# Performance work log

Measured on AMD Instinct MI355X. Metric: run time of the kernel, lower is better.

Reference implementation:

```python
import jax, jax.numpy as jnp
import numpy as np

B, T, D, H = 4, 2048, 1024, 16
HD = D // H  # 64


def setup_inputs() -> dict:
    key = jax.random.key(0)
    k1, k2, k3 = jax.random.split(key, 3)
    x = jax.random.normal(k1, (B, T, D), dtype=jnp.float32)
    # xavier-uniform-ish scaling for stability
    W_qkv = jax.random.normal(k2, (3 * D, D), dtype=jnp.float32) * (1.0 / np.sqrt(D))
    W_proj = jax.random.normal(k3, (D, D), dtype=jnp.float32) * (1.0 / np.sqrt(D))
    b_proj = jnp.zeros((D,), dtype=jnp.float32)
    return {"x": x, "W_qkv": W_qkv, "W_proj": W_proj, "b_proj": b_proj}


def reference(x, W_qkv, W_proj, b_proj):
    Bx, Tx, C = x.shape
    qkv = x @ W_qkv.T                      # [B,T,3C]
    q, k, v = jnp.split(qkv, 3, axis=-1)
    # [B,T,C] -> [B,H,T,hd]
    def heads(t):
        return t.reshape(Bx, Tx, H, HD).transpose(0, 2, 1, 3)
    q, k, v = heads(q), heads(k), heads(v)
    scale = 1.0 / np.sqrt(HD)
    scores = jnp.einsum('bhqd,bhkd->bhqk', q, k) * scale  # [B,H,T,T]
    causal = jnp.tril(jnp.ones((Tx, Tx), dtype=bool))
    scores = jnp.where(causal, scores, jnp.finfo(scores.dtype).min)
    attn = jax.nn.softmax(scores, axis=-1)
    out = jnp.einsum('bhqk,bhkd->bhqd', attn, v)          # [B,H,T,hd]
    out = out.transpose(0, 2, 1, 3).reshape(Bx, Tx, C)    # [B,T,C]
    return out @ W_proj.T + b_proj
```

## Files before the change

### kernel.cpp

```cpp
#include <hip/hip_runtime.h>
#include <hip/hip_bf16.h>

#define B_  4
#define T_  2048
#define D_  1024
#define H_  16
#define HD_ 64
#define THREE_D (3 * D_)
#define TWO_D   (2 * D_)

typedef short s16x8 __attribute__((ext_vector_type(8)));
typedef float f32x4 __attribute__((ext_vector_type(4)));
typedef unsigned short u16;
typedef unsigned short u16x4 __attribute__((ext_vector_type(4)));

static __device__ __forceinline__ s16x8 load8(const u16* p) {
    return *reinterpret_cast<const s16x8*>(p);
}
static __device__ __forceinline__ u16 f2bf(float f) {
    __hip_bfloat16 h = __float2bfloat16(f);
    return *reinterpret_cast<u16*>(&h);
}
static __device__ __forceinline__ u16 bftrunc(float f) {
    unsigned u; __builtin_memcpy(&u, &f, 4); return (u16)(u >> 16);
}

static __device__ __forceinline__ void gload_lds16(const u16* g, u16* l) {
#if __has_builtin(__builtin_amdgcn_global_load_lds)
    __builtin_amdgcn_global_load_lds(
        (__attribute__((address_space(1))) void*)g,
        (__attribute__((address_space(3))) void*)l, 16, 0, 0);
#else
    *reinterpret_cast<s16x8*>(l) = load8(g);
#endif
}

__global__ __launch_bounds__(256) void cvt_f32_bf16(
    const float* __restrict__ in, u16* __restrict__ out, int n)
{
    const int i = (blockIdx.x * 256 + threadIdx.x) * 4;
    if (i < n) {
        const float4 f = *reinterpret_cast<const float4*>(in + i);
        u16x4 r;
        r.x = f2bf(f.x); r.y = f2bf(f.y); r.z = f2bf(f.z); r.w = f2bf(f.w);
        *reinterpret_cast<u16x4*>(out + i) = r;
    }
}

template<int MODE>
__global__ __launch_bounds__(256) void gemm_bt128(
    const u16* __restrict__ A,
    const u16* __restrict__ Bm,
    void* __restrict__ Cv,
    const float* __restrict__ bias,
    int M, int N, int K, int lda, int ldb, int ldc,
    float qsc, u16* __restrict__ vt)
{
    const int ntiles = N >> 7;
    const int mt = blockIdx.x / ntiles;
    const int nt = blockIdx.x % ntiles;
    const int m0 = mt * 128, n0 = nt * 128;
    const int tid  = threadIdx.x;
    const int lane = tid & 63;
    const int l15  = lane & 15;
    const int quad = lane >> 4;
    const int wave = tid >> 6;
    const int wm = (wave >> 1) * 64;
    const int wn = (wave & 1) * 64;

    __shared__ u16 A_sh[2][128 * 32];
    __shared__ u16 B_sh[2][128 * 32];

    f32x4 acc[4][4] = {};

    const int c0 = tid, c1 = tid + 256;
    const int ar0 = c0 >> 2, as0 = (c0 & 3) * 8;
    const int ar1 = c1 >> 2, as1 = (c1 & 3) * 8;
    const u16* Ag0 = A  + (size_t)(m0 + ar0) * lda + as0;
    const u16* Ag1 = A  + (size_t)(m0 + ar1) * lda + as1;
    const u16* Bg0 = Bm + (size_t)(n0 + ar0) * ldb + as0;
    const u16* Bg1 = Bm + (size_t)(n0 + ar1) * ldb + as1;

    for (int k0 = 0; k0 < K; k0 += 64) {
        __syncthreads();
        #pragma unroll
        for (int p = 0; p < 2; ++p) {
            gload_lds16(Ag0 + k0 + p * 32, &A_sh[p][c0 * 8]);
            gload_lds16(Ag1 + k0 + p * 32, &A_sh[p][c1 * 8]);
            gload_lds16(Bg0 + k0 + p * 32, &B_sh[p][c0 * 8]);
            gload_lds16(Bg1 + k0 + p * 32, &B_sh[p][c1 * 8]);
        }
        __syncthreads();

        #pragma unroll
        for (int p = 0; p < 2; ++p) {
            s16x8 a[4], b[4];
            #pragma unroll
            for (int i = 0; i < 4; ++i) {
                a[i] = *reinterpret_cast<const s16x8*>(&A_sh[p][(wm + i * 16 + l15) * 32 + quad * 8]);
                b[i] = *reinterpret_cast<const s16x8*>(&B_sh[p][(wn + i * 16 + l15) * 32 + quad * 8]);
            }
            #pragma unroll
            for (int mi = 0; mi < 4; ++mi)
                #pragma unroll
                for (int ni = 0; ni < 4; ++ni)
                    acc[mi][ni] = __builtin_amdgcn_mfma_f32_16x16x32_bf16(
                        a[mi], b[ni], acc[mi][ni], 0, 0, 0);
        }
    }

    #pragma unroll
    for (int ni = 0; ni < 4; ++ni) {
        const int col = n0 + wn + ni * 16 + l15;
        if (MODE == 0) {
            const float bv = bias ? bias[col] : 0.0f;
            #pragma unroll
            for (int mi = 0; mi < 4; ++mi) {
                const int row = m0 + wm + mi * 16 + quad * 4;
                #pragma unroll
                for (int r = 0; r < 4; ++r)
                    ((float*)Cv)[(size_t)(row + r) * ldc + col] = acc[mi][ni][r] + bv;
            }
        } else {
            if (col < TWO_D) {
                const float sc = (col < D_) ? qsc : 1.0f;
                #pragma unroll
                for (int mi = 0; mi < 4; ++mi) {
                    const int row = m0 + wm + mi * 16 + quad * 4;
                    #pragma unroll
                    for (int r = 0; r < 4; ++r)
                        ((u16*)Cv)[(size_t)(row + r) * ldc + col] = f2bf(acc[mi][ni][r] * sc);
                }
            } else {
                const int vc = col - TWO_D;
                #pragma unroll
                for (int mi = 0; mi < 4; ++mi) {
                    const int row = m0 + wm + mi * 16 + quad * 4;
                    const int bb = row >> 11, t = row & (T_ - 1);
                    u16x4 pk;
                    #pragma unroll
                    for (int r = 0; r < 4; ++r) pk[r] = f2bf(acc[mi][ni][r]);
                    *reinterpret_cast<u16x4*>(
                        vt + ((size_t)(bb * H_ * HD_) + vc) * T_ + t) = pk;
                }
            }
        }
    }
}

__global__ __launch_bounds__(256) void flash_attn6(
    const u16* __restrict__ qk, const u16* __restrict__ vt,
    u16* __restrict__ out)
{
    const int cls = blockIdx.x >> 6;
    const int bh  = blockIdx.x & 63;
    const int qmap[16] = {15,14,13,12, 8,9,10,11, 7,6,5,4, 0,1,2,3};
    const int qt = qmap[cls];
    const int h = bh & 15, b = bh >> 4;
    const int q0 = qt * 128;

    __shared__ u16 K_lds[64 * 72];
    __shared__ u16 V_lds[64 * 72];
    __shared__ u16 P_lds[4 * 32 * 72];

    const int tid = threadIdx.x;
    const int wave = tid >> 6, lane = tid & 63;
    const int l15 = lane & 15, quad = lane >> 4;
    u16* Pw = P_lds + wave * (32 * 72);

    const int w0 = q0 + wave * 32;

    s16x8 qf[2][2];
    #pragma unroll
    for (int mi = 0; mi < 2; ++mi) {
        const size_t rowQ = (size_t)(b * T_ + w0 + mi * 16 + l15) * TWO_D + h * HD_;
        qf[mi][0] = load8(qk + rowQ + quad * 8);
        qf[mi][1] = load8(qk + rowQ + 32 + quad * 8);
    }

    f32x4 o[2][4] = {};
    f32x4 osum[2] = {};

    s16x8 ones;
    #pragma unroll
    for (int j = 0; j < 8; ++j) ones[j] = (short)0x3F80;

    const int r0 = tid >> 3;
    const int s0 = (tid & 7) * 8;
    const u16* Kg0 = qk + (size_t)(b * T_ + r0)      * TWO_D + D_ + h * HD_ + s0;
    const u16* Kg1 = qk + (size_t)(b * T_ + r0 + 32) * TWO_D + D_ + h * HD_ + s0;
    const u16* Vg0 = vt + (size_t)(bh * HD_ + r0)      * T_ + s0;
    const u16* Vg1 = vt + (size_t)(bh * HD_ + r0 + 32) * T_ + s0;

    s16x8 pk0 = load8(Kg0);
    s16x8 pk1 = load8(Kg1);
    s16x8 pv0 = load8(Vg0);
    s16x8 pv1 = load8(Vg1);

    const int nkt = 2 * qt + 2;
    for (int kt = 0; kt < nkt; ++kt) {
        const int kbase = kt * 64;
        __syncthreads();
        *reinterpret_cast<s16x8*>(&K_lds[r0 * 72 + s0])        = pk0;
        *reinterpret_cast<s16x8*>(&K_lds[(r0 + 32) * 72 + s0]) = pk1;
        *reinterpret_cast<s16x8*>(&V_lds[r0 * 72 + s0])        = pv0;
        *reinterpret_cast<s16x8*>(&V_lds[(r0 + 32) * 72 + s0]) = pv1;
        __syncthreads();

        if (kt + 1 < nkt) {
            const int nb = kbase + 64;
            pk0 = load8(Kg0 + (size_t)nb * TWO_D);
            pk1 = load8(Kg1 + (size_t)nb * TWO_D);
            pv0 = load8(Vg0 + nb);
            pv1 = load8(Vg1 + nb);
        }

        if (kbase <= w0 + 31) {
            f32x4 st[2][4];
            #pragma unroll
            for (int n = 0; n < 4; ++n) {
                const s16x8 kf0 = *reinterpret_cast<const s16x8*>(
                    &K_lds[(n * 16 + l15) * 72 + quad * 8]);
                const s16x8 kf1 = *reinterpret_cast<const s16x8*>(
                    &K_lds[(n * 16 + l15) * 72 + 32 + quad * 8]);
                #pragma unroll
                for (int mi = 0; mi < 2; ++mi) {
                    f32x4 t = {};
                    t = __builtin_amdgcn_mfma_f32_16x16x32_bf16(kf0, qf[mi][0], t, 0, 0, 0);
                    t = __builtin_amdgcn_mfma_f32_16x16x32_bf16(kf1, qf[mi][1], t, 0, 0, 0);
                    st[mi][n] = t;
                }
            }

            const bool diag = (kbase + 63 > w0);
            #pragma unroll
            for (int mi = 0; mi < 2; ++mi) {
                const int qr = w0 + mi * 16 + l15;
                #pragma unroll
                for (int n = 0; n < 4; ++n) {
                    const int kb = kbase + n * 16 + quad * 4;
                    u16x4 pk;
                    #pragma unroll
                    for (int r = 0; r < 4; ++r)
                        pk[r] = bftrunc(exp2f(st[mi][n][r]));
                    if (diag) {
                        #pragma unroll
                        for (int r = 0; r < 4; ++r)
                            if (kb + r > qr) pk[r] = 0;
                    }
                    *reinterpret_cast<u16x4*>(
                        &Pw[(mi * 16 + l15) * 72 + n * 16 + quad * 4]) = pk;
                }
            }

            #pragma unroll
            for (int ks = 0; ks < 2; ++ks) {
                s16x8 pa[2];
                #pragma unroll
                for (int mi = 0; mi < 2; ++mi) {
                    pa[mi] = *reinterpret_cast<const s16x8*>(
                        &Pw[(mi * 16 + l15) * 72 + ks * 32 + quad * 8]);
                    osum[mi] = __builtin_amdgcn_mfma_f32_16x16x32_bf16(
                        pa[mi], ones, osum[mi], 0, 0, 0);
                }
                #pragma unroll
                for (int n4 = 0; n4 < 4; ++n4) {
                    const s16x8 vb = *reinterpret_cast<const s16x8*>(
                        &V_lds[(n4 * 16 + l15) * 72 + ks * 32 + quad * 8]);
                    #pragma unroll
                    for (int mi = 0; mi < 2; ++mi)
                        o[mi][n4] = __builtin_amdgcn_mfma_f32_16x16x32_bf16(
                            pa[mi], vb, o[mi][n4], 0, 0, 0);
                }
            }
        }
    }

    #pragma unroll
    for (int mi = 0; mi < 2; ++mi)
        #pragma unroll
        for (int r = 0; r < 4; ++r) {
            const float inv = 1.0f / osum[mi][r];
            const size_t rowO = (size_t)(b * T_ + w0 + mi * 16 + quad * 4 + r) * D_ + h * HD_;
            #pragma unroll
            for (int n4 = 0; n4 < 4; ++n4)
                out[rowO + n4 * 16 + l15] = f2bf(o[mi][n4][r] * inv);
        }
}

extern "C" void kernel_launch(void* const* d_in, const int* in_sizes, int n_in,
                              void* d_out, int out_size, void* d_ws, size_t ws_size,
                              hipStream_t stream)
{
    const float* x     = (const float*)d_in[0];
    const float* Wqkv  = (const float*)d_in[1];
    const float* Wproj = (const float*)d_in[2];
    const float* bproj = (const float*)d_in[3];
    float* out = (float*)d_out;

    const int M = B_ * T_;
    const float cs = 0.18033688011f;

    u16* xb    = (u16*)d_ws;
    u16* wqkvb = xb    + (size_t)M * D_;
    u16* wprob = wqkvb + (size_t)THREE_D * D_;
    u16* qk    = wprob + (size_t)D_ * D_;
    u16* vtb   = qk    + (size_t)M * TWO_D;
    u16* attn  = vtb   + (size_t)B_ * H_ * HD_ * T_;

    {
        int n;
        n = M * D_;
        cvt_f32_bf16<<<dim3((n / 4 + 255) / 256), 256, 0, stream>>>(x, xb, n);
        n = THREE_D * D_;
        cvt_f32_bf16<<<dim3((n / 4 + 255) / 256), 256, 0, stream>>>(Wqkv, wqkvb, n);
        n = D_ * D_;
        cvt_f32_bf16<<<dim3((n / 4 + 255) / 256), 256, 0, stream>>>(Wproj, wprob, n);
    }

    gemm_bt128<1><<<dim3((M / 128) * (THREE_D / 128)), 256, 0, stream>>>(
        xb, wqkvb, qk, nullptr, M, THREE_D, D_, D_, D_, TWO_D, cs, vtb);

    flash_attn6<<<dim3(B_ * H_ * (T_ / 128)), 256, 0, stream>>>(qk, vtb, attn);

    gemm_bt128<0><<<dim3((M / 128) * (D_ / 128)), 256, 0, stream>>>(
        attn, wprob, out, bproj, M, D_, D_, D_, D_, D_, 1.0f, nullptr);
}
```

Baseline: 255.6 us.

## Rework attention kernel with 32x32 MFMA, register-resident P, and async double-buffered K/V

```diff
diff --git a/kernel.cpp b/kernel.cpp
--- a/kernel.cpp
+++ b/kernel.cpp
@@ -11,6 +11,8 @@
 
 typedef short s16x8 __attribute__((ext_vector_type(8)));
 typedef float f32x4 __attribute__((ext_vector_type(4)));
+typedef float f32x16 __attribute__((ext_vector_type(16)));
+typedef unsigned int u32x4 __attribute__((ext_vector_type(4)));
 typedef unsigned short u16;
 typedef unsigned short u16x4 __attribute__((ext_vector_type(4)));
 
@@ -21,8 +23,13 @@
     __hip_bfloat16 h = __float2bfloat16(f);
     return *reinterpret_cast<u16*>(&h);
 }
-static __device__ __forceinline__ u16 bftrunc(float f) {
-    unsigned u; __builtin_memcpy(&u, &f, 4); return (u16)(u >> 16);
+static __device__ __forceinline__ unsigned cvtpk(float lo, float hi) {
+    float2 f; f.x = lo; f.y = hi;
+    __hip_bfloat162 h = __float22bfloat162_rn(f);
+    return *reinterpret_cast<unsigned*>(&h);
+}
+static __device__ __forceinline__ void swap32(unsigned& a, unsigned& b) {
+    asm("v_permlane32_swap_b32 %0, %1" : "+v"(a), "+v"(b));
 }
 
 static __device__ __forceinline__ void gload_lds16(const u16* g, u16* l) {
@@ -148,7 +155,7 @@
     }
 }
 
-__global__ __launch_bounds__(256) void flash_attn6(
+__global__ __launch_bounds__(256) void flash_attn7(
     const u16* __restrict__ qk, const u16* __restrict__ vt,
     u16* __restrict__ out)
 {
@@ -156,136 +163,129 @@
     const int bh  = blockIdx.x & 63;
     const int qmap[16] = {15,14,13,12, 8,9,10,11, 7,6,5,4, 0,1,2,3};
     const int qt = qmap[cls];
-    const int h = bh & 15, b = bh >> 4;
+    const int hh = bh & 15, b = bh >> 4;
     const int q0 = qt * 128;
 
-    __shared__ u16 K_lds[64 * 72];
-    __shared__ u16 V_lds[64 * 72];
-    __shared__ u16 P_lds[4 * 32 * 72];
+    __shared__ u16 K_lds[2][64 * 64];
+    __shared__ u16 V_lds[2][64 * 64];
 
     const int tid = threadIdx.x;
     const int wave = tid >> 6, lane = tid & 63;
-    const int l15 = lane & 15, quad = lane >> 4;
-    u16* Pw = P_lds + wave * (32 * 72);
-
+    const int l31 = lane & 31, half = lane >> 5;
+    const int sw = (l31 & 7) << 4;
     const int w0 = q0 + wave * 32;
-
-    s16x8 qf[2][2];
-    #pragma unroll
-    for (int mi = 0; mi < 2; ++mi) {
-        const size_t rowQ = (size_t)(b * T_ + w0 + mi * 16 + l15) * TWO_D + h * HD_;
-        qf[mi][0] = load8(qk + rowQ + quad * 8);
-        qf[mi][1] = load8(qk + rowQ + 32 + quad * 8);
-    }
-
-    f32x4 o[2][4] = {};
-    f32x4 osum[2] = {};
+    const int qr = w0 + l31;
+
+    s16x8 qf[4];
+    {
+        const size_t rowQ = (size_t)(b * T_ + w0 + l31) * TWO_D + hh * HD_;
+        #pragma unroll
+        for (int s = 0; s < 4; ++s)
+            qf[s] = load8(qk + rowQ + s * 16 + half * 8);
+    }
+
+    f32x16 o[2] = {};
+    f32x16 osum = {};
 
     s16x8 ones;
     #pragma unroll
     for (int j = 0; j < 8; ++j) ones[j] = (short)0x3F80;
 
     const int r0 = tid >> 3;
-    const int s0 = (tid & 7) * 8;
-    const u16* Kg0 = qk + (size_t)(b * T_ + r0)      * TWO_D + D_ + h * HD_ + s0;
-    const u16* Kg1 = qk + (size_t)(b * T_ + r0 + 32) * TWO_D + D_ + h * HD_ + s0;
-    const u16* Vg0 = vt + (size_t)(bh * HD_ + r0)      * T_ + s0;
-    const u16* Vg1 = vt + (size_t)(bh * HD_ + r0 + 32) * T_ + s0;
-
-    s16x8 pk0 = load8(Kg0);
-    s16x8 pk1 = load8(Kg1);
-    s16x8 pv0 = load8(Vg0);
-    s16x8 pv1 = load8(Vg1);
+    const int ch = tid & 7;
+    const int scol = ((ch * 16) ^ ((r0 & 7) << 4)) >> 1;
+    const u16* Kg = qk + (size_t)(b * T_ + r0) * TWO_D + D_ + hh * HD_ + scol;
+    const u16* Vg = vt + (size_t)(bh * HD_ + r0) * T_ + scol;
+
+#define STAGE(bf, kb64) do {                                                  \
+        const size_t ko = (size_t)(kb64) * TWO_D;                             \
+        gload_lds16(Kg + ko,                       &K_lds[bf][(size_t)tid * 8]);        \
+        gload_lds16(Kg + ko + (size_t)32 * TWO_D,  &K_lds[bf][(size_t)(tid + 256) * 8]);\
+        gload_lds16(Vg + (kb64),                   &V_lds[bf][(size_t)tid * 8]);        \
+        gload_lds16(Vg + (kb64) + (size_t)32 * T_, &V_lds[bf][(size_t)(tid + 256) * 8]);\
+    } while (0)
 
     const int nkt = 2 * qt + 2;
+    STAGE(0, 0);
+    int cur = 0;
+
     for (int kt = 0; kt < nkt; ++kt) {
         const int kbase = kt * 64;
         __syncthreads();
-        *reinterpret_cast<s16x8*>(&K_lds[r0 * 72 + s0])        = pk0;
-        *reinterpret_cast<s16x8*>(&K_lds[(r0 + 32) * 72 + s0]) = pk1;
-        *reinterpret_cast<s16x8*>(&V_lds[r0 * 72 + s0])        = pv0;
-        *reinterpret_cast<s16x8*>(&V_lds[(r0 + 32) * 72 + s0]) = pv1;
-        __syncthreads();
-
-        if (kt + 1 < nkt) {
-            const int nb = kbase + 64;
-            pk0 = load8(Kg0 + (size_t)nb * TWO_D);
-            pk1 = load8(Kg1 + (size_t)nb * TWO_D);
-            pv0 = load8(Vg0 + nb);
-            pv1 = load8(Vg1 + nb);
+        if (kt + 1 < nkt) STAGE(cur ^ 1, (kt + 1) * 64);
+
+        if (kbase <= w0 + 31) {
+            const char* Kb = (const char*)&K_lds[cur][0];
+            const char* Vb = (const char*)&V_lds[cur][0];
+
+            f32x16 st[2];
+            #pragma unroll
+            for (int kb = 0; kb < 2; ++kb) {
+                f32x16 acc = {};
+                #pragma unroll
+                for (int s = 0; s < 4; ++s) {
+                    const s16x8 kf = *reinterpret_cast<const s16x8*>(
+                        Kb + (kb * 32 + l31) * 128 + ((s * 32 + half * 16) ^ sw));
+                    acc = __builtin_amdgcn_mfma_f32_32x32x16_bf16(
+                        kf, qf[s], acc, 0, 0, 0);
+                }
+                st[kb] = acc;
+            }
+
+            const bool diag = (kbase + 63 > w0);
+            float p[2][16];
+            #pragma unroll
+            for (int kb = 0; kb < 2; ++kb)
+                #pragma unroll
+                for (int r = 0; r < 16; ++r) {
+                    float e = exp2f(st[kb][r]);
+                    if (diag) {
+                        const int key = kbase + kb * 32 + (r & 3) + 8 * (r >> 2) + 4 * half;
+                        if (key > qr) e = 0.0f;
+                    }
+                    p[kb][r] = e;
+                }
+
+            s16x8 pa[4];
+            #pragma unroll
+            for (int kb = 0; kb < 2; ++kb)
+                #pragma unroll
+                for (int t = 0; t < 2; ++t) {
+                    unsigned a  = cvtpk(p[kb][8 * t + 0], p[kb][8 * t + 1]);
+                    unsigned bq = cvtpk(p[kb][8 * t + 4], p[kb][8 * t + 5]);
+                    unsigned c  = cvtpk(p[kb][8 * t + 2], p[kb][8 * t + 3]);
+                    unsigned d  = cvtpk(p[kb][8 * t + 6], p[kb][8 * t + 7]);
+                    swap32(a, bq);
+                    swap32(c, d);
+                    u32x4 w; w.x = a; w.y = c; w.z = bq; w.w = d;
+                    pa[kb * 2 + t] = __builtin_bit_cast(s16x8, w);
+                }
+
+            #pragma unroll
+            for (int s = 0; s < 4; ++s) {
+                osum = __builtin_amdgcn_mfma_f32_32x32x16_bf16(
+                    pa[s], ones, osum, 0, 0, 0);
+                #pragma unroll
+                for (int fb = 0; fb < 2; ++fb) {
+                    const s16x8 vb = *reinterpret_cast<const s16x8*>(
+                        Vb + (fb * 32 + l31) * 128 + ((s * 32 + half * 16) ^ sw));
+                    o[fb] = __builtin_amdgcn_mfma_f32_32x32x16_bf16(
+                        pa[s], vb, o[fb], 0, 0, 0);
+                }
+            }
         }
-
-        if (kbase <= w0 + 31) {
-            f32x4 st[2][4];
-            #pragma unroll
-            for (int n = 0; n < 4; ++n) {
-                const s16x8 kf0 = *reinterpret_cast<const s16x8*>(
-                    &K_lds[(n * 16 + l15) * 72 + quad * 8]);
-                const s16x8 kf1 = *reinterpret_cast<const s16x8*>(
-                    &K_lds[(n * 16 + l15) * 72 + 32 + quad * 8]);
-                #pragma unroll
-                for (int mi = 0; mi < 2; ++mi) {
-                    f32x4 t = {};
-                    t = __builtin_amdgcn_mfma_f32_16x16x32_bf16(kf0, qf[mi][0], t, 0, 0, 0);
-                    t = __builtin_amdgcn_mfma_f32_16x16x32_bf16(kf1, qf[mi][1], t, 0, 0, 0);
-                    st[mi][n] = t;
-                }
-            }
-
-            const bool diag = (kbase + 63 > w0);
-            #pragma unroll
-            for (int mi = 0; mi < 2; ++mi) {
-                const int qr = w0 + mi * 16 + l15;
-                #pragma unroll
-                for (int n = 0; n < 4; ++n) {
-                    const int kb = kbase + n * 16 + quad * 4;
-                    u16x4 pk;
-                    #pragma unroll
-                    for (int r = 0; r < 4; ++r)
-                        pk[r] = bftrunc(exp2f(st[mi][n][r]));
-                    if (diag) {
-                        #pragma unroll
-                        for (int r = 0; r < 4; ++r)
-                            if (kb + r > qr) pk[r] = 0;
-                    }
-                    *reinterpret_cast<u16x4*>(
-                        &Pw[(mi * 16 + l15) * 72 + n * 16 + quad * 4]) = pk;
-                }
-            }
-
-            #pragma unroll
-            for (int ks = 0; ks < 2; ++ks) {
-                s16x8 pa[2];
-                #pragma unroll
-                for (int mi = 0; mi < 2; ++mi) {
-                    pa[mi] = *reinterpret_cast<const s16x8*>(
-                        &Pw[(mi * 16 + l15) * 72 + ks * 32 + quad * 8]);
-                    osum[mi] = __builtin_amdgcn_mfma_f32_16x16x32_bf16(
-                        pa[mi], ones, osum[mi], 0, 0, 0);
-                }
-                #pragma unroll
-                for (int n4 = 0; n4 < 4; ++n4) {
-                    const s16x8 vb = *reinterpret_cast<const s16x8*>(
-                        &V_lds[(n4 * 16 + l15) * 72 + ks * 32 + quad * 8]);
-                    #pragma unroll
-                    for (int mi = 0; mi < 2; ++mi)
-                        o[mi][n4] = __builtin_amdgcn_mfma_f32_16x16x32_bf16(
-                            pa[mi], vb, o[mi][n4], 0, 0, 0);
-                }
-            }
-        }
-    }
+        cur ^= 1;
+    }
+#undef STAGE
 
     #pragma unroll
-    for (int mi = 0; mi < 2; ++mi)
-        #pragma unroll
-        for (int r = 0; r < 4; ++r) {
-            const float inv = 1.0f / osum[mi][r];
-            const size_t rowO = (size_t)(b * T_ + w0 + mi * 16 + quad * 4 + r) * D_ + h * HD_;
-            #pragma unroll
-            for (int n4 = 0; n4 < 4; ++n4)
-                out[rowO + n4 * 16 + l15] = f2bf(o[mi][n4][r] * inv);
-        }
+    for (int r = 0; r < 16; ++r) {
+        const int qrow = w0 + (r & 3) + 8 * (r >> 2) + 4 * half;
+        const float inv = 1.0f / osum[r];
+        const size_t ro = (size_t)(b * T_ + qrow) * D_ + hh * HD_;
+        out[ro + l31]      = f2bf(o[0][r] * inv);
+        out[ro + 32 + l31] = f2bf(o[1][r] * inv);
+    }
 }
 
 extern "C" void kernel_launch(void* const* d_in, const int* in_sizes, int n_in,
@@ -321,7 +321,7 @@
     gemm_bt128<1><<<dim3((M / 128) * (THREE_D / 128)), 256, 0, stream>>>(
         xb, wqkvb, qk, nullptr, M, THREE_D, D_, D_, D_, TWO_D, cs, vtb);
 
-    flash_attn6<<<dim3(B_ * H_ * (T_ / 128)), 256, 0, stream>>>(qk, vtb, attn);
+    flash_attn7<<<dim3(B_ * H_ * (T_ / 128)), 256, 0, stream>>>(qk, vtb, attn);
 
     gemm_bt128<0><<<dim3((M / 128) * (D_ / 128)), 256, 0, stream>>>(
         attn, wprob, out, bproj, M, D_, D_, D_, D_, D_, 1.0f, nullptr);
```

Result: slower. 272.1 us (+6.5%).

## Keep softmax probabilities in registers using 16x16x16 MFMA instead of LDS round-trip

Applied to the files above, without the earlier changes.

```diff
diff --git a/kernel.cpp b/kernel.cpp
--- a/kernel.cpp
+++ b/kernel.cpp
@@ -10,7 +10,9 @@
 #define TWO_D   (2 * D_)
 
 typedef short s16x8 __attribute__((ext_vector_type(8)));
+typedef short s16x4 __attribute__((ext_vector_type(4)));
 typedef float f32x4 __attribute__((ext_vector_type(4)));
+typedef unsigned int u32x2 __attribute__((ext_vector_type(2)));
 typedef unsigned short u16;
 typedef unsigned short u16x4 __attribute__((ext_vector_type(4)));
 
@@ -21,8 +23,22 @@
     __hip_bfloat16 h = __float2bfloat16(f);
     return *reinterpret_cast<u16*>(&h);
 }
-static __device__ __forceinline__ u16 bftrunc(float f) {
-    unsigned u; __builtin_memcpy(&u, &f, 4); return (u16)(u >> 16);
+static __device__ __forceinline__ unsigned cvtpk(float lo, float hi) {
+    float2 f; f.x = lo; f.y = hi;
+    __hip_bfloat162 h = __float22bfloat162_rn(f);
+    return *reinterpret_cast<unsigned*>(&h);
+}
+static __device__ __forceinline__ void mfma16(f32x4& d, u16x4 a, u16x4 b) {
+#if __has_builtin(__builtin_amdgcn_mfma_f32_16x16x16bf16_1k)
+    d = __builtin_amdgcn_mfma_f32_16x16x16bf16_1k(
+        __builtin_bit_cast(s16x4, a), __builtin_bit_cast(s16x4, b), d, 0, 0, 0);
+#else
+    asm volatile("s_nop 1\n\t"
+                 "v_mfma_f32_16x16x16_bf16 %0, %1, %2, %0\n\t"
+                 "s_nop 7\n\t"
+                 "s_nop 3"
+                 : "+v"(d) : "v"(a), "v"(b));
+#endif
 }
 
 static __device__ __forceinline__ void gload_lds16(const u16* g, u16* l) {
@@ -148,7 +164,7 @@
     }
 }
 
-__global__ __launch_bounds__(256) void flash_attn6(
+__global__ __launch_bounds__(256) void flash_attn9(
     const u16* __restrict__ qk, const u16* __restrict__ vt,
     u16* __restrict__ out)
 {
@@ -161,12 +177,10 @@
 
     __shared__ u16 K_lds[64 * 72];
     __shared__ u16 V_lds[64 * 72];
-    __shared__ u16 P_lds[4 * 32 * 72];
 
     const int tid = threadIdx.x;
     const int wave = tid >> 6, lane = tid & 63;
     const int l15 = lane & 15, quad = lane >> 4;
-    u16* Pw = P_lds + wave * (32 * 72);
 
     const int w0 = q0 + wave * 32;
 
@@ -181,9 +195,9 @@
     f32x4 o[2][4] = {};
     f32x4 osum[2] = {};
 
-    s16x8 ones;
+    u16x4 ones4;
     #pragma unroll
-    for (int j = 0; j < 8; ++j) ones[j] = (short)0x3F80;
+    for (int j = 0; j < 4; ++j) ones4[j] = 0x3F80;
 
     const int r0 = tid >> 3;
     const int s0 = (tid & 7) * 8;
@@ -233,44 +247,40 @@
             }
 
             const bool diag = (kbase + 63 > w0);
+            u16x4 pa[2][4];
             #pragma unroll
             for (int mi = 0; mi < 2; ++mi) {
                 const int qr = w0 + mi * 16 + l15;
                 #pragma unroll
                 for (int n = 0; n < 4; ++n) {
                     const int kb = kbase + n * 16 + quad * 4;
-                    u16x4 pk;
-                    #pragma unroll
-                    for (int r = 0; r < 4; ++r)
-                        pk[r] = bftrunc(exp2f(st[mi][n][r]));
+                    float e0 = exp2f(st[mi][n][0]);
+                    float e1 = exp2f(st[mi][n][1]);
+                    float e2 = exp2f(st[mi][n][2]);
+                    float e3 = exp2f(st[mi][n][3]);
                     if (diag) {
-                        #pragma unroll
-                        for (int r = 0; r < 4; ++r)
-                            if (kb + r > qr) pk[r] = 0;
+                        if (kb + 0 > qr) e0 = 0.0f;
+                        if (kb + 1 > qr) e1 = 0.0f;
+                        if (kb + 2 > qr) e2 = 0.0f;
+                        if (kb + 3 > qr) e3 = 0.0f;
                     }
-                    *reinterpret_cast<u16x4*>(
-                        &Pw[(mi * 16 + l15) * 72 + n * 16 + quad * 4]) = pk;
-                }
-            }
-
-            #pragma unroll
-            for (int ks = 0; ks < 2; ++ks) {
-                s16x8 pa[2];
-                #pragma unroll
-                for (int mi = 0; mi < 2; ++mi) {
-                    pa[mi] = *reinterpret_cast<const s16x8*>(
-                        &Pw[(mi * 16 + l15) * 72 + ks * 32 + quad * 8]);
-                    osum[mi] = __builtin_amdgcn_mfma_f32_16x16x32_bf16(
-                        pa[mi], ones, osum[mi], 0, 0, 0);
-                }
+                    u32x2 w; w.x = cvtpk(e0, e1); w.y = cvtpk(e2, e3);
+                    pa[mi][n] = __builtin_bit_cast(u16x4, w);
+                }
+            }
+
+            #pragma unroll
+            for (int n = 0; n < 4; ++n) {
+                #pragma unroll
+                for (int mi = 0; mi < 2; ++mi)
+                    mfma16(osum[mi], pa[mi][n], ones4);
                 #pragma unroll
                 for (int n4 = 0; n4 < 4; ++n4) {
-                    const s16x8 vb = *reinterpret_cast<const s16x8*>(
-                        &V_lds[(n4 * 16 + l15) * 72 + ks * 32 + quad * 8]);
+                    const u16x4 vb = *reinterpret_cast<const u16x4*>(
+                        &V_lds[(n4 * 16 + l15) * 72 + n * 16 + quad * 4]);
                     #pragma unroll
                     for (int mi = 0; mi < 2; ++mi)
-                        o[mi][n4] = __builtin_amdgcn_mfma_f32_16x16x32_bf16(
-                            pa[mi], vb, o[mi][n4], 0, 0, 0);
+                        mfma16(o[mi][n4], pa[mi][n], vb);
                 }
             }
         }
@@ -321,7 +331,7 @@
     gemm_bt128<1><<<dim3((M / 128) * (THREE_D / 128)), 256, 0, stream>>>(
         xb, wqkvb, qk, nullptr, M, THREE_D, D_, D_, D_, TWO_D, cs, vtb);
 
-    flash_attn6<<<dim3(B_ * H_ * (T_ / 128)), 256, 0, stream>>>(qk, vtb, attn);
+    flash_attn9<<<dim3(B_ * H_ * (T_ / 128)), 256, 0, stream>>>(qk, vtb, attn);
 
     gemm_bt128<0><<<dim3((M / 128) * (D_ / 128)), 256, 0, stream>>>(
         attn, wprob, out, bproj, M, D_, D_, D_, D_, D_, 1.0f, nullptr);
```

Result: slower. 266.1 us (+4.1%).

## Use 256x256-tile pipelined GEMM with XCD-aware block remap for QKV projection

Applied to the files above, without the earlier changes.

```diff
diff --git a/kernel.cpp b/kernel.cpp
--- a/kernel.cpp
+++ b/kernel.cpp
@@ -44,6 +44,161 @@
         u16x4 r;
         r.x = f2bf(f.x); r.y = f2bf(f.y); r.z = f2bf(f.z); r.w = f2bf(f.w);
         *reinterpret_cast<u16x4*>(out + i) = r;
+    }
+}
+
+__global__ __launch_bounds__(512, 2) void gemm256_qkv(
+    const u16* __restrict__ A, const u16* __restrict__ Bm,
+    u16* __restrict__ Cq, u16* __restrict__ vt,
+    float qsc, int M, int N, int K, int lda, int ldb)
+{
+    const int ntiles = N >> 8;
+    const int nwg = (M >> 8) * ntiles;
+    const int cpx = nwg >> 3;
+    const int wg = ((int)blockIdx.x & 7) * cpx + ((int)blockIdx.x >> 3);
+    const int mt = wg / ntiles, nt = wg % ntiles;
+    const int m0 = mt << 8, n0 = nt << 8;
+
+    const int tid  = threadIdx.x;
+    const int lane = tid & 63;
+    const int l15  = lane & 15;
+    const int quad = lane >> 4;
+    const int wave = tid >> 6;
+    const int wm2  = wave >> 2;
+    const int wn4  = wave & 3;
+
+    __shared__ u16 Ash[2][256 * 64];
+    __shared__ u16 Bsh[2][256 * 64];
+
+    f32x4 acc[8][4] = {};
+
+    const int srow = tid >> 3;
+    const int scol = ((tid & 7) * 8) ^ ((srow & 4) ? 16 : 0);
+    const u16* Ag = A  + (size_t)(m0 + srow) * lda + scol;
+    const u16* Bg = Bm + (size_t)(n0 + srow) * ldb + scol;
+
+#define STAGE_A(buf, kt, h) do {                                             \
+        gload_lds16(Ag + (size_t)(2*(h))   * 64 * lda + (size_t)(kt) * 64,   \
+                    &Ash[buf][((size_t)tid + (2*(h))   * 512) * 8]);         \
+        gload_lds16(Ag + (size_t)(2*(h)+1) * 64 * lda + (size_t)(kt) * 64,   \
+                    &Ash[buf][((size_t)tid + (2*(h)+1) * 512) * 8]);         \
+    } while (0)
+#define STAGE_B(buf, kt, h) do {                                             \
+        gload_lds16(Bg + (size_t)(2*(h))   * 64 * ldb + (size_t)(kt) * 64,   \
+                    &Bsh[buf][((size_t)tid + (2*(h))   * 512) * 8]);         \
+        gload_lds16(Bg + (size_t)(2*(h)+1) * 64 * ldb + (size_t)(kt) * 64,   \
+                    &Bsh[buf][((size_t)tid + (2*(h)+1) * 512) * 8]);         \
+    } while (0)
+
+    s16x8 bf[4][2];
+#define LOAD_B(buf) do {                                                     \
+        _Pragma("unroll")                                                    \
+        for (int nf = 0; nf < 4; ++nf) {                                     \
+            const int row = wn4 * 64 + nf * 16 + l15;                        \
+            const int cs_ = (row & 4) ? 16 : 0;                              \
+            bf[nf][0] = *reinterpret_cast<const s16x8*>(                     \
+                &Bsh[buf][row * 64 + ((quad * 8) ^ cs_)]);                   \
+            bf[nf][1] = *reinterpret_cast<const s16x8*>(                     \
+                &Bsh[buf][row * 64 + ((32 + quad * 8) ^ cs_)]);              \
+        }                                                                    \
+    } while (0)
+#define MFMA_PAIR(buf, MF0) do {                                             \
+        __builtin_amdgcn_s_setprio(1);                                       \
+        _Pragma("unroll")                                                    \
+        for (int dm = 0; dm < 2; ++dm) {                                     \
+            const int mf = (MF0) + dm;                                       \
+            const int row = wm2 * 128 + mf * 16 + l15;                       \
+            const int cs_ = (row & 4) ? 16 : 0;                              \
+            const s16x8 a0 = *reinterpret_cast<const s16x8*>(                \
+                &Ash[buf][row * 64 + ((quad * 8) ^ cs_)]);                   \
+            const s16x8 a1 = *reinterpret_cast<const s16x8*>(                \
+                &Ash[buf][row * 64 + ((32 + quad * 8) ^ cs_)]);              \
+            _Pragma("unroll")                                                \
+            for (int nf = 0; nf < 4; ++nf) {                                 \
+                acc[mf][nf] = __builtin_amdgcn_mfma_f32_16x16x32_bf16(       \
+                    a0, bf[nf][0], acc[mf][nf], 0, 0, 0);                    \
+                acc[mf][nf] = __builtin_amdgcn_mfma_f32_16x16x32_bf16(       \
+                    a1, bf[nf][1], acc[mf][nf], 0, 0, 0);                    \
+            }                                                                \
+        }                                                                    \
+        __builtin_amdgcn_s_setprio(0);                                       \
+    } while (0)
+
+    STAGE_A(0, 0, 0); STAGE_A(0, 0, 1); STAGE_B(0, 0, 0); STAGE_B(0, 0, 1);
+
+    const int nkt = K >> 6;
+    const int niter = K >> 7;
+    for (int it = 0; it < niter; ++it) {
+        const int t1 = 2 * it + 1;
+        const int t2 = (2 * it + 2) & (nkt - 1);
+        STAGE_A(1, t1, 0);
+        asm volatile("s_waitcnt vmcnt(2)" ::: "memory");
+        __builtin_amdgcn_s_barrier();
+        LOAD_B(0);
+        MFMA_PAIR(0, 0);
+        __builtin_amdgcn_s_barrier();
+
+        STAGE_A(1, t1, 1);
+        MFMA_PAIR(0, 2);
+        __builtin_amdgcn_s_barrier();
+
+        STAGE_B(1, t1, 0);
+        MFMA_PAIR(0, 4);
+        __builtin_amdgcn_s_barrier();
+
+        STAGE_B(1, t1, 1);
+        MFMA_PAIR(0, 6);
+        __builtin_amdgcn_s_barrier();
+
+        STAGE_A(0, t2, 0);
+        asm volatile("s_waitcnt vmcnt(2)" ::: "memory");
+        __builtin_amdgcn_s_barrier();
+        LOAD_B(1);
+        MFMA_PAIR(1, 0);
+        __builtin_amdgcn_s_barrier();
+
+        STAGE_A(0, t2, 1);
+        MFMA_PAIR(1, 2);
+        __builtin_amdgcn_s_barrier();
+
+        STAGE_B(0, t2, 0);
+        MFMA_PAIR(1, 4);
+        __builtin_amdgcn_s_barrier();
+
+        STAGE_B(0, t2, 1);
+        MFMA_PAIR(1, 6);
+        __builtin_amdgcn_s_barrier();
+    }
+#undef STAGE_A
+#undef STAGE_B
+#undef LOAD_B
+#undef MFMA_PAIR
+
+    #pragma unroll
+    for (int nf = 0; nf < 4; ++nf) {
+        const int col = n0 + wn4 * 64 + nf * 16 + l15;
+        if (col < TWO_D) {
+            const float sc = (col < D_) ? qsc : 1.0f;
+            #pragma unroll
+            for (int mf = 0; mf < 8; ++mf) {
+                const int row = m0 + wm2 * 128 + mf * 16 + quad * 4;
+                #pragma unroll
+                for (int r = 0; r < 4; ++r)
+                    Cq[(size_t)(row + r) * TWO_D + col] = f2bf(acc[mf][nf][r] * sc);
+            }
+        } else {
+            const int vc = col - TWO_D;
+            #pragma unroll
+            for (int mf = 0; mf < 8; ++mf) {
+                const int row = m0 + wm2 * 128 + mf * 16 + quad * 4;
+                const int bb = row >> 11, t = row & (T_ - 1);
+                u16x4 pk;
+                #pragma unroll
+                for (int r = 0; r < 4; ++r) pk[r] = f2bf(acc[mf][nf][r]);
+                *reinterpret_cast<u16x4*>(
+                    vt + ((size_t)(bb * H_ * HD_) + vc) * T_ + t) = pk;
+            }
+        }
     }
 }
 
@@ -318,8 +473,8 @@
         cvt_f32_bf16<<<dim3((n / 4 + 255) / 256), 256, 0, stream>>>(Wproj, wprob, n);
     }
 
-    gemm_bt128<1><<<dim3((M / 128) * (THREE_D / 128)), 256, 0, stream>>>(
-        xb, wqkvb, qk, nullptr, M, THREE_D, D_, D_, D_, TWO_D, cs, vtb);
+    gemm256_qkv<<<dim3((M / 256) * (THREE_D / 256)), 512, 0, stream>>>(
+        xb, wqkvb, qk, vtb, cs, M, THREE_D, D_, D_, D_);
 
     flash_attn6<<<dim3(B_ * H_ * (T_ / 128)), 256, 0, stream>>>(qk, vtb, attn);
 
```

Result: slower. 270.1 us (+5.7%).
